# Kernel tuning notes

Measured on AMD Instinct MI355X. Metric: run time of the kernel, lower is better.

## Reference

```python
import jax, jax.numpy as jnp
import numpy as np

TEMP = 1.0
B, FLAT, K, D = 8, 262144, 256, 4  # FLAT = M*D, M = 65536


def setup_inputs() -> dict:
    key = jax.random.key(0)
    k1, k2 = jax.random.split(key)
    x = jax.random.normal(k1, (B, FLAT), dtype=jnp.float32)
    center = jax.random.normal(k2, (K, D), dtype=jnp.float32)
    return {"x": x, "center": center}


def reference(x, center):
    # Soft vector quantization (Q_type='Soft')
    x_ = x.reshape(x.shape[0], -1, D)                      # [B, M, 4]
    # sim = -||x - c||^2, expanded to avoid [B,M,K,4] intermediate
    x_sq = jnp.sum(x_ * x_, axis=-1, keepdims=True)        # [B, M, 1]
    c_sq = jnp.sum(center * center, axis=-1)               # [K]
    xc = jnp.einsum('bmd,kd->bmk', x_, center)             # [B, M, K]
    sim = -(x_sq - 2.0 * xc + c_sq)                        # [B, M, K]
    smx = jax.nn.softmax(TEMP * sim, axis=-1)              # [B, M, K]
    output = jnp.einsum('bmk,kd->bmd', smx, center)        # [B, M, 4]
    return output.reshape(x.shape)
```

## Files before the change

### kernel.cpp

```cpp
#include <hip/hip_runtime.h>
#include <hip/hip_bf16.h>

#ifndef __has_builtin
#define __has_builtin(x) 0
#endif

typedef __attribute__((ext_vector_type(8))) short short8;
typedef __attribute__((ext_vector_type(4))) float floatx4;

__device__ __forceinline__ float fast_exp2(float x) {
#if __has_builtin(__builtin_amdgcn_exp2f)
    return __builtin_amdgcn_exp2f(x);
#else
    return exp2f(x);
#endif
}
__device__ __forceinline__ float fast_rcp(float x) {
#if __has_builtin(__builtin_amdgcn_rcpf)
    return __builtin_amdgcn_rcpf(x);
#else
    return 1.0f / x;
#endif
}
__device__ __forceinline__ unsigned short bf16_of(float v) {
    union { __hip_bfloat16 b; unsigned short s; } cv;
    cv.b = __float2bfloat16(v);
    return cv.s;
}
__device__ __forceinline__ float bf16_back(unsigned short s) {
    union { __hip_bfloat16 b; unsigned short t; } cv;
    cv.t = s;
    return __bfloat162float(cv.b);
}
__device__ __forceinline__ unsigned bcat(unsigned short lo, unsigned short hi) {
    return (unsigned)lo | ((unsigned)hi << 16);
}
__device__ __forceinline__ unsigned pack_bf16(float a, float b) {
    __hip_bfloat162 h = __float22bfloat162_rn(make_float2(a, b));
    union { __hip_bfloat162 h2; unsigned u; } cv;
    cv.h2 = h;
    return cv.u;
}

#define VQ_K 256
#define BLK  1024
#define T    4


__global__ void vq_prep(const float* __restrict__ center, uint4* __restrict__ ws) {
    const float L2E = 1.4426950408889634f;
    int f = blockIdx.x * 256 + threadIdx.x;
    if (f < 512) {
        int lane32 = f & 31;
        int q  = lane32 >> 4;
        int ml = lane32 & 15;
        int k  = (f >> 5) * 16 + ml;
        float4 c = reinterpret_cast<const float4*>(center)[k];
        float s = 2.0f * L2E;
        float c2f[4] = {s * c.x, s * c.y, s * c.z, s * c.w};
        unsigned short ch[4], cl[4];
#pragma unroll
        for (int d = 0; d < 4; ++d) {
            ch[d] = bf16_of(c2f[d]);
            cl[d] = bf16_of(c2f[d] - bf16_back(ch[d]));
        }
        float b = -L2E * (c.x * c.x + c.y * c.y + c.z * c.z + c.w * c.w);
        unsigned short bh = bf16_of(b);
        unsigned short bl = bf16_of(b - bf16_back(bh));
        uint4 e;
        if (q == 0) {
            e.x = bcat(ch[0], ch[1]); e.y = bcat(ch[2], ch[3]);
            e.z = e.x;                e.w = e.y;
        } else {
            e.x = bcat(cl[0], cl[1]); e.y = bcat(cl[2], cl[3]);
            e.z = bcat(bh, bl);       e.w = 0;
        }
        ws[f] = e;
    } else {
        int g = f - 512;
        int c = g >> 6, q = (g >> 4) & 3, n = g & 15;
        unsigned rr[4];
#pragma unroll
        for (int r = 0; r < 4; ++r) {
            int j0 = 2 * r, j1 = 2 * r + 1;
            int k0 = 32 * c + (j0 < 4 ? 4 * q + j0 : 16 + 4 * q + j0 - 4);
            int k1 = 32 * c + (j1 < 4 ? 4 * q + j1 : 16 + 4 * q + j1 - 4);
            float v0 = (n < 4) ? center[k0 * 4 + n] : (n == 4 ? 1.f : 0.f);
            float v1 = (n < 4) ? center[k1 * 4 + n] : (n == 4 ? 1.f : 0.f);
            rr[r] = bcat(bf16_of(v0), bf16_of(v1));
        }
        ws[f] = make_uint4(rr[0], rr[1], rr[2], rr[3]);
    }
}

__global__ __launch_bounds__(BLK, 8) void vq_main(const float* __restrict__ x,
                                                  const uint4* __restrict__ ws,
                                                  float* __restrict__ out) {
    const int lane = threadIdx.x & 63;
    const int wv   = threadIdx.x >> 6;
    const int q    = lane >> 4;
    const int ml   = lane & 15;
    const int mbase = blockIdx.x * (16 * 16 * T) + wv * (16 * T);
    const float4* __restrict__ x4 = reinterpret_cast<const float4*>(x);
    const uint4* __restrict__ ta = ws;
    const uint4* __restrict__ tv = ws + 512;

    union Frag { uint4 u4; unsigned u[4]; short8 v; };

    Frag B[T];
#pragma unroll
    for (int t = 0; t < T; ++t) {
        float4 xv = x4[mbase + t * 16 + ml];
        float xf[4] = {xv.x, xv.y, xv.z, xv.w};
        unsigned short xh[4], xl[4];
#pragma unroll
        for (int d = 0; d < 4; ++d) {
            xh[d] = bf16_of(xf[d]);
            xl[d] = bf16_of(xf[d] - bf16_back(xh[d]));
        }
        unsigned h01 = bcat(xh[0], xh[1]), h23 = bcat(xh[2], xh[3]);
        unsigned l01 = bcat(xl[0], xl[1]), l23 = bcat(xl[2], xl[3]);
        const unsigned ONE2 = 0x3F803F80u;
        B[t].u[0] = (q <= 1) ? h01 : 0;
        B[t].u[1] = (q <= 1) ? h23 : 0;
        B[t].u[2] = (q == 0) ? l01 : ((q == 1) ? ONE2 : 0);
        B[t].u[3] = (q == 0) ? l23 : 0;
    }

    floatx4 O[T];
#pragma unroll
    for (int t = 0; t < T; ++t) O[t] = (floatx4){0.f, 0.f, 0.f, 0.f};
    const floatx4 Z4 = (floatx4){0.f, 0.f, 0.f, 0.f};

    for (int c = 0; c < 8; ++c) {
        Frag a0, a1, vf;
        a0.u4 = make_uint4(0u, 0u, 0u, 0u);
        a1.u4 = make_uint4(0u, 0u, 0u, 0u);
        if (q < 2) {
            a0.u4 = ta[(2 * c) * 32 + (lane & 31)];
            a1.u4 = ta[(2 * c + 1) * 32 + (lane & 31)];
        }
        vf.u4 = tv[c * 64 + lane];
#pragma unroll
        for (int t = 0; t < T; ++t) {
            floatx4 S0 = __builtin_amdgcn_mfma_f32_16x16x32_bf16(a0.v, B[t].v, Z4, 0, 0, 0);
            floatx4 S1 = __builtin_amdgcn_mfma_f32_16x16x32_bf16(a1.v, B[t].v, Z4, 0, 0, 0);
            Frag p;
            p.u[0] = pack_bf16(fast_exp2(S0[0]), fast_exp2(S0[1]));
            p.u[1] = pack_bf16(fast_exp2(S0[2]), fast_exp2(S0[3]));
            p.u[2] = pack_bf16(fast_exp2(S1[0]), fast_exp2(S1[1]));
            p.u[3] = pack_bf16(fast_exp2(S1[2]), fast_exp2(S1[3]));
            O[t] = __builtin_amdgcn_mfma_f32_16x16x32_bf16(p.v, vf.v, O[t], 0, 0, 0);
        }
    }

#pragma unroll
    for (int t = 0; t < T; ++t) {
#pragma unroll
        for (int r = 0; r < 4; ++r) {
            float den = __shfl(O[t][r], (lane & 48) + 4, 64);
            float val = O[t][r] * fast_rcp(den);
            int m = mbase + t * 16 + q * 4 + r;
            if (ml < 4) out[m * 4 + ml] = val;
        }
    }
}

extern "C" void kernel_launch(void* const* d_in, const int* in_sizes, int n_in,
                              void* d_out, int out_size, void* d_ws, size_t ws_size,
                              hipStream_t stream) {
    const float* x      = (const float*)d_in[0];
    const float* center = (const float*)d_in[1];
    float* out = (float*)d_out;
    uint4* ws  = (uint4*)d_ws;

    vq_prep<<<4, 256, 0, stream>>>(center, ws);

    int nvec   = in_sizes[0] / 4;
    int blocks = nvec / (16 * 16 * T);
    vq_main<<<blocks, BLK, 0, stream>>>(x, ws, out);
}
```

Baseline: 83.65 us.

## Fuse center-table preparation into main kernel via shared memory

Removes the separate prep kernel launch and builds the bf16 center/value tables per block in LDS before the main loop, reading them from shared memory instead of global workspace. This eliminates one kernel launch and the inter-kernel dependency, at the cost of every block redundantly recomputing the 16KB table and adding a __syncthreads. The LDS use (16KB per block) may limit occupancy relative to the launch-bounds target.

```diff
diff --git a/kernel.cpp b/kernel.cpp
--- a/kernel.cpp
+++ b/kernel.cpp
@@ -47,63 +47,66 @@
 #define T    4
 
 
-__global__ void vq_prep(const float* __restrict__ center, uint4* __restrict__ ws) {
-    const float L2E = 1.4426950408889634f;
-    int f = blockIdx.x * 256 + threadIdx.x;
-    if (f < 512) {
-        int lane32 = f & 31;
-        int q  = lane32 >> 4;
-        int ml = lane32 & 15;
-        int k  = (f >> 5) * 16 + ml;
-        float4 c = reinterpret_cast<const float4*>(center)[k];
-        float s = 2.0f * L2E;
-        float c2f[4] = {s * c.x, s * c.y, s * c.z, s * c.w};
-        unsigned short ch[4], cl[4];
+__global__ __launch_bounds__(BLK, 8) void vq_main(const float* __restrict__ x,
+                                                  const float* __restrict__ center,
+                                                  float* __restrict__ out) {
+    __shared__ uint4 tbl[1024];
+
+    {
+        const float L2E = 1.4426950408889634f;
+        int f = threadIdx.x;
+        if (f < 512) {
+            int lane32 = f & 31;
+            int qq = lane32 >> 4;
+            int mm = lane32 & 15;
+            int k  = (f >> 5) * 16 + mm;
+            float4 c = reinterpret_cast<const float4*>(center)[k];
+            float s = 2.0f * L2E;
+            float c2f[4] = {s * c.x, s * c.y, s * c.z, s * c.w};
+            unsigned short ch[4], cl[4];
 #pragma unroll
-        for (int d = 0; d < 4; ++d) {
-            ch[d] = bf16_of(c2f[d]);
-            cl[d] = bf16_of(c2f[d] - bf16_back(ch[d]));
+            for (int d = 0; d < 4; ++d) {
+                ch[d] = bf16_of(c2f[d]);
+                cl[d] = bf16_of(c2f[d] - bf16_back(ch[d]));
+            }
+            float b = -L2E * (c.x * c.x + c.y * c.y + c.z * c.z + c.w * c.w);
+            unsigned short bh = bf16_of(b);
+            unsigned short bl = bf16_of(b - bf16_back(bh));
+            uint4 e;
+            if (qq == 0) {
+                e.x = bcat(ch[0], ch[1]); e.y = bcat(ch[2], ch[3]);
+                e.z = e.x;                e.w = e.y;
+            } else {
+                e.x = bcat(cl[0], cl[1]); e.y = bcat(cl[2], cl[3]);
+                e.z = bcat(bh, bl);       e.w = 0;
+            }
+            tbl[f] = e;
+        } else {
+            int g = f - 512;
+            int c = g >> 6, qq = (g >> 4) & 3, n = g & 15;
+            unsigned rr[4];
+#pragma unroll
+            for (int r = 0; r < 4; ++r) {
+                int j0 = 2 * r, j1 = 2 * r + 1;
+                int k0 = 32 * c + (j0 < 4 ? 4 * qq + j0 : 16 + 4 * qq + j0 - 4);
+                int k1 = 32 * c + (j1 < 4 ? 4 * qq + j1 : 16 + 4 * qq + j1 - 4);
+                float v0 = (n < 4) ? center[k0 * 4 + n] : (n == 4 ? 1.f : 0.f);
+                float v1 = (n < 4) ? center[k1 * 4 + n] : (n == 4 ? 1.f : 0.f);
+                rr[r] = bcat(bf16_of(v0), bf16_of(v1));
+            }
+            tbl[f] = make_uint4(rr[0], rr[1], rr[2], rr[3]);
         }
-        float b = -L2E * (c.x * c.x + c.y * c.y + c.z * c.z + c.w * c.w);
-        unsigned short bh = bf16_of(b);
-        unsigned short bl = bf16_of(b - bf16_back(bh));
-        uint4 e;
-        if (q == 0) {
-            e.x = bcat(ch[0], ch[1]); e.y = bcat(ch[2], ch[3]);
-            e.z = e.x;                e.w = e.y;
-        } else {
-            e.x = bcat(cl[0], cl[1]); e.y = bcat(cl[2], cl[3]);
-            e.z = bcat(bh, bl);       e.w = 0;
-        }
-        ws[f] = e;
-    } else {
-        int g = f - 512;
-        int c = g >> 6, q = (g >> 4) & 3, n = g & 15;
-        unsigned rr[4];
-#pragma unroll
-        for (int r = 0; r < 4; ++r) {
-            int j0 = 2 * r, j1 = 2 * r + 1;
-            int k0 = 32 * c + (j0 < 4 ? 4 * q + j0 : 16 + 4 * q + j0 - 4);
-            int k1 = 32 * c + (j1 < 4 ? 4 * q + j1 : 16 + 4 * q + j1 - 4);
-            float v0 = (n < 4) ? center[k0 * 4 + n] : (n == 4 ? 1.f : 0.f);
-            float v1 = (n < 4) ? center[k1 * 4 + n] : (n == 4 ? 1.f : 0.f);
-            rr[r] = bcat(bf16_of(v0), bf16_of(v1));
-        }
-        ws[f] = make_uint4(rr[0], rr[1], rr[2], rr[3]);
     }
-}
+    __syncthreads();
 
-__global__ __launch_bounds__(BLK, 8) void vq_main(const float* __restrict__ x,
-                                                  const uint4* __restrict__ ws,
-                                                  float* __restrict__ out) {
     const int lane = threadIdx.x & 63;
     const int wv   = threadIdx.x >> 6;
     const int q    = lane >> 4;
     const int ml   = lane & 15;
     const int mbase = blockIdx.x * (16 * 16 * T) + wv * (16 * T);
     const float4* __restrict__ x4 = reinterpret_cast<const float4*>(x);
-    const uint4* __restrict__ ta = ws;
-    const uint4* __restrict__ tv = ws + 512;
+    const uint4* ta = tbl;
+    const uint4* tv = tbl + 512;
 
     union Frag { uint4 u4; unsigned u[4]; short8 v; };
 
@@ -172,11 +175,9 @@
     const float* x      = (const float*)d_in[0];
     const float* center = (const float*)d_in[1];
     float* out = (float*)d_out;
-    uint4* ws  = (uint4*)d_ws;
-
-    vq_prep<<<4, 256, 0, stream>>>(center, ws);
+    (void)d_ws; (void)ws_size;
 
     int nvec   = in_sizes[0] / 4;
     int blocks = nvec / (16 * 16 * T);
-    vq_main<<<blocks, BLK, 0, stream>>>(x, ws, out);
+    vq_main<<<blocks, BLK, 0, stream>>>(x, center, out);
 }
```

Result: no change. 82.11 us (-1.8%).
